# Optimization experiments

Hardware: AMD Instinct MI355X
Metric: run time of the kernel (lower is better)

The kernel has to match this reference:

```python
import jax, jax.numpy as jnp
import numpy as np

KH, KW, STRIDE = 5, 5, 1
OUT_CH = 64


def setup_inputs() -> dict:
    key = jax.random.key(0)
    k1, k2 = jax.random.split(key)
    x = jax.random.normal(k1, (16, 1, 256, 256), dtype=jnp.float32)
    # kaiming_uniform_(a=sqrt(5)) on fan_in=25 gives bound ~= sqrt(6/((1+5)*25)) ~= 0.2
    w = jax.random.uniform(k2, (OUT_CH, 1, KH, KW), dtype=jnp.float32, minval=-0.2, maxval=0.2)
    w = w.at[0].set(0.0)  # reset_parameters zeroes the first filter
    return {"x": x, "weight": w}


def reference(x, weight):
    """Faithful vectorized RBF_Conv2d forward.

    Original: for each output pixel (k,l), cdist between the flattened window
    (B, kh*kw) and flattened weights (O, kh*kw), std = sample std (ddof=1) of
    the (B,O) distance matrix, output = gauss(dist, std) = exp(-0.5*(d/std)^2).
    """
    B = x.shape[0]
    O = weight.shape[0]
    # im2col: (B, P=kh*kw, Ho, Wo), valid padding (in_channels == 1)
    patches = jax.lax.conv_general_dilated_patches(
        x, (KH, KW), (STRIDE, STRIDE), 'VALID')
    wf = weight.reshape(O, -1)                                  # (O, P)
    pn = jnp.sum(patches * patches, axis=1)                     # (B, Ho, Wo)
    wn = jnp.sum(wf * wf, axis=1)                               # (O,)
    cross = jnp.einsum('bphw,op->bohw', patches, wf)            # (B, O, Ho, Wo)
    d2 = pn[:, None] + wn[None, :, None, None] - 2.0 * cross
    dist = jnp.sqrt(jnp.maximum(d2, 1e-12))                     # euclidean cdist
    # per-output-pixel sample std (ddof=1) over the (B, O) distance matrix
    mean = jnp.mean(dist, axis=(0, 1), keepdims=True)           # (1,1,Ho,Wo)
    var = jnp.sum((dist - mean) ** 2, axis=(0, 1), keepdims=True) / (B * O - 1)
    std = jnp.sqrt(var)
    # gauss RBF
    return jnp.exp(-0.5 * (dist / std) ** 2)
```

## Files before the change

kernel.cpp:

```cpp
#include <hip/hip_runtime.h>

typedef float v2f __attribute__((ext_vector_type(2)));

#define KH 5
#define KW 5
#define HH 256
#define WW 256
#define HO 252
#define WO 252
#define NB 16
#define NO 64
#define PLANE (HO * WO)
#define NPASS 5
#define XC 85

__global__ __launch_bounds__(512, 4)
void rbf_conv2d_kernel(const float* __restrict__ x, const float* __restrict__ w,
                       float* __restrict__ out) {
    __shared__ float xs[NB][KH][XC];
    __shared__ float wn[NO];
    __shared__ float pS1[2][8][16];
    __shared__ float pS2[2][8][16];

    const int t  = threadIdx.x;
    const int k  = blockIdx.y;
    const int a0 = (4 * k) & 31;
    const int Le = a0 - 64 + 64 * (int)blockIdx.x;
    if (Le - 16 >= WO || Le + 64 <= 0) return;
    const int colbase = Le - 16;

    for (int idx = t; idx < NB * KH * XC; idx += 512) {
        int b   = idx / (KH * XC);
        int rem = idx - b * (KH * XC);
        int r   = rem / XC;
        int c   = rem - r * XC;
        int col = colbase + c;
        col = col < 0 ? 0 : (col > WW - 1 ? WW - 1 : col);
        xs[b][r][c] = x[(b * HH + k + r) * WW + col];
    }
    if (t < NO) {
        float s = 0.f;
        #pragma unroll
        for (int i = 0; i < 25; ++i) { float v = w[t * 25 + i]; s = fmaf(v, v, s); }
        wn[t] = s;
    }
    __syncthreads();

    const int p     = t & 15;
    const int b     = (t >> 4) & 15;
    const int obase = __builtin_amdgcn_readfirstlane((t >> 8) << 5);
    const int wv    = t >> 6;
    const int lane  = t & 63;
    const int bo_base = ((b * NO + obase) * HO + k) * WO;

    #pragma unroll 1
    for (int pi = 0; pi < NPASS; ++pi) {
        const int  Lp     = colbase + 16 * pi;
        const bool active = (Lp + 16 > 0) && (Lp < WO);
        const int  pb     = pi & 1;

        v2f   dv[16];
        float s1 = 0.f, s2 = 0.f;

        if (active) {
            float pr[25];
            float pn = 0.f;
            #pragma unroll
            for (int r = 0; r < KH; ++r)
                #pragma unroll
                for (int c = 0; c < KW; ++c) {
                    float v = xs[b][r][16 * pi + p + c];
                    pr[r * KW + c] = v;
                    pn = fmaf(v, v, pn);
                }
            v2f prv[12];
            #pragma unroll
            for (int i = 0; i < 12; ++i) { prv[i].x = pr[2 * i]; prv[i].y = pr[2 * i + 1]; }
            const float pr24 = pr[24];

            #pragma unroll
            for (int j = 0; j < 16; ++j) {
                float cr0, cr1;
                {
                    const float* __restrict__ wr = w + (obase + 2 * j) * 25;
                    v2f acc = {0.f, 0.f};
                    #pragma unroll
                    for (int i = 0; i < 12; ++i) {
                        v2f wv_; wv_.x = wr[2 * i]; wv_.y = wr[2 * i + 1];
                        acc = __builtin_elementwise_fma(prv[i], wv_, acc);
                    }
                    cr0 = acc.x + acc.y + pr24 * wr[24];
                }
                {
                    const float* __restrict__ wr = w + (obase + 2 * j + 1) * 25;
                    v2f acc = {0.f, 0.f};
                    #pragma unroll
                    for (int i = 0; i < 12; ++i) {
                        v2f wv_; wv_.x = wr[2 * i]; wv_.y = wr[2 * i + 1];
                        acc = __builtin_elementwise_fma(prv[i], wv_, acc);
                    }
                    cr1 = acc.x + acc.y + pr24 * wr[24];
                }
                float d20 = fmaxf(fmaf(-2.f, cr0, pn + wn[obase + 2 * j]),     1e-12f);
                float d21 = fmaxf(fmaf(-2.f, cr1, pn + wn[obase + 2 * j + 1]), 1e-12f);
                s2 += d20 + d21;
                dv[j].x = __builtin_amdgcn_sqrtf(d20);
                dv[j].y = __builtin_amdgcn_sqrtf(d21);
                s1 += dv[j].x + dv[j].y;
            }

            s1 += __shfl_xor(s1, 16); s2 += __shfl_xor(s2, 16);
            s1 += __shfl_xor(s1, 32); s2 += __shfl_xor(s2, 32);
            if (lane < 16) { pS1[pb][wv][lane] = s1; pS2[pb][wv][lane] = s2; }
        }
        __syncthreads();

        if (active) {
            float S1 = 0.f, S2 = 0.f;
            #pragma unroll
            for (int q = 0; q < 8; ++q) { S1 += pS1[pb][q][p]; S2 += pS2[pb][q][p]; }
            const float var  = (S2 - S1 * S1 * (1.0f / 1024.0f)) * (1.0f / 1023.0f);
            const float cinv = -0.72134752044448170368f / var;

            const int  l   = Lp + p;
            const bool ok  = (l >= 0) && (l < WO);
            const bool okE = ok && (pi >= 1);
            const bool okO = ok && (pi <= 3);
            v2f cv; cv.x = cinv; cv.y = cinv;
            const int base = bo_base + l;
            #pragma unroll
            for (int j = 0; j < 16; ++j) {
                v2f tt = dv[j] * dv[j];
                tt = tt * cv;
                float e0 = exp2f(tt.x);
                float e1 = exp2f(tt.y);
                if (okE) out[base + (2 * j) * PLANE]     = e0;
                if (okO) out[base + (2 * j + 1) * PLANE] = e1;
            }
        }
    }
}

extern "C" void kernel_launch(void* const* d_in, const int* in_sizes, int n_in,
                              void* d_out, int out_size, void* d_ws, size_t ws_size,
                              hipStream_t stream) {
    const float* x = (const float*)d_in[0];
    const float* w = (const float*)d_in[1];
    float* out = (float*)d_out;
    dim3 grid(6, HO);
    rbf_conv2d_kernel<<<grid, 512, 0, stream>>>(x, w, out);
}
```

Measured before the change: 349.5 us.

## Recompute distances in a second pass instead of holding them in registers

Restructures the kernel so each thread owns one output column across all 64 output channels and two batch elements, in place of the old 16-column passes. It makes two passes: the first computes the distance sums for the per-pixel std, and the second recomputes the 25-tap dot products and writes exp2 results directly. This removes the 16-entry distance register array and the overlapping passes with their partial writes, lowering register pressure and producing 64-lane contiguous stores. The cost is roughly double the FMA work for the cross terms and a different tile mapping with a smaller grid.

After: 340.2 us. -2.7%, faster.

```diff
diff --git a/kernel.cpp b/kernel.cpp
--- a/kernel.cpp
+++ b/kernel.cpp
@@ -11,30 +11,30 @@
 #define NB 16
 #define NO 64
 #define PLANE (HO * WO)
-#define NPASS 5
-#define XC 85
+#define TLW 64
+#define XCOLS (TLW + KW - 1)
 
 __global__ __launch_bounds__(512, 4)
 void rbf_conv2d_kernel(const float* __restrict__ x, const float* __restrict__ w,
                        float* __restrict__ out) {
-    __shared__ float xs[NB][KH][XC];
+    __shared__ float xs[NB][KH][XCOLS];
     __shared__ float wn[NO];
-    __shared__ float pS1[2][8][16];
-    __shared__ float pS2[2][8][16];
+    __shared__ float pS1[8][TLW];
+    __shared__ float pS2[8][TLW];
+    __shared__ float cinv_s[TLW];
 
-    const int t  = threadIdx.x;
-    const int k  = blockIdx.y;
-    const int a0 = (4 * k) & 31;
-    const int Le = a0 - 64 + 64 * (int)blockIdx.x;
-    if (Le - 16 >= WO || Le + 64 <= 0) return;
-    const int colbase = Le - 16;
+    const int t = threadIdx.x;
+    const int k = blockIdx.y;
+    const int a = (4 * k) & 15;
+    const int l0 = a - TLW + TLW * (int)blockIdx.x;
+    if (l0 >= WO || l0 + TLW <= 0) return;
 
-    for (int idx = t; idx < NB * KH * XC; idx += 512) {
-        int b   = idx / (KH * XC);
-        int rem = idx - b * (KH * XC);
-        int r   = rem / XC;
-        int c   = rem - r * XC;
-        int col = colbase + c;
+    for (int idx = t; idx < NB * KH * XCOLS; idx += 512) {
+        int b   = idx / (KH * XCOLS);
+        int rem = idx - b * (KH * XCOLS);
+        int r   = rem / XCOLS;
+        int c   = rem - r * XCOLS;
+        int col = l0 + c;
         col = col < 0 ? 0 : (col > WW - 1 ? WW - 1 : col);
         xs[b][r][c] = x[(b * HH + k + r) * WW + col];
     }
@@ -46,96 +46,124 @@
     }
     __syncthreads();
 
-    const int p     = t & 15;
-    const int b     = (t >> 4) & 15;
-    const int obase = __builtin_amdgcn_readfirstlane((t >> 8) << 5);
-    const int wv    = t >> 6;
-    const int lane  = t & 63;
-    const int bo_base = ((b * NO + obase) * HO + k) * WO;
+    const int lane = t & 63;
+    const int bg   = __builtin_amdgcn_readfirstlane(t >> 6);
+    const int l    = l0 + lane;
 
+    float s1 = 0.f, s2 = 0.f;
     #pragma unroll 1
-    for (int pi = 0; pi < NPASS; ++pi) {
-        const int  Lp     = colbase + 16 * pi;
-        const bool active = (Lp + 16 > 0) && (Lp < WO);
-        const int  pb     = pi & 1;
+    for (int bi = 0; bi < 2; ++bi) {
+        const int b = bg + 8 * bi;
+        float pr[25];
+        float pn = 0.f;
+        #pragma unroll
+        for (int r = 0; r < KH; ++r)
+            #pragma unroll
+            for (int c = 0; c < KW; ++c) {
+                float v = xs[b][r][lane + c];
+                pr[r * KW + c] = v;
+                pn = fmaf(v, v, pn);
+            }
+        v2f prv[12];
+        #pragma unroll
+        for (int i = 0; i < 12; ++i) { prv[i].x = pr[2 * i]; prv[i].y = pr[2 * i + 1]; }
+        const float pr24 = pr[24];
 
-        v2f   dv[16];
-        float s1 = 0.f, s2 = 0.f;
+        #pragma unroll 8
+        for (int j = 0; j < 32; ++j) {
+            float cr0, cr1;
+            {
+                const float* __restrict__ wr = w + (2 * j) * 25;
+                v2f acc = {0.f, 0.f};
+                #pragma unroll
+                for (int i = 0; i < 12; ++i) {
+                    v2f wv_; wv_.x = wr[2 * i]; wv_.y = wr[2 * i + 1];
+                    acc = __builtin_elementwise_fma(prv[i], wv_, acc);
+                }
+                cr0 = acc.x + acc.y + pr24 * wr[24];
+            }
+            {
+                const float* __restrict__ wr = w + (2 * j + 1) * 25;
+                v2f acc = {0.f, 0.f};
+                #pragma unroll
+                for (int i = 0; i < 12; ++i) {
+                    v2f wv_; wv_.x = wr[2 * i]; wv_.y = wr[2 * i + 1];
+                    acc = __builtin_elementwise_fma(prv[i], wv_, acc);
+                }
+                cr1 = acc.x + acc.y + pr24 * wr[24];
+            }
+            v2f wn2 = *(const v2f*)&wn[2 * j];
+            float d20 = fmaxf(fmaf(-2.f, cr0, pn + wn2.x), 1e-12f);
+            float d21 = fmaxf(fmaf(-2.f, cr1, pn + wn2.y), 1e-12f);
+            s2 += d20 + d21;
+            s1 += __builtin_amdgcn_sqrtf(d20) + __builtin_amdgcn_sqrtf(d21);
+        }
+    }
+    pS1[bg][lane] = s1;
+    pS2[bg][lane] = s2;
+    __syncthreads();
 
-        if (active) {
-            float pr[25];
-            float pn = 0.f;
+    if (t < TLW) {
+        float S1 = 0.f, S2 = 0.f;
+        #pragma unroll
+        for (int q = 0; q < 8; ++q) { S1 += pS1[q][t]; S2 += pS2[q][t]; }
+        const float var = (S2 - S1 * S1 * (1.0f / 1024.0f)) * (1.0f / 1023.0f);
+        cinv_s[t] = -0.72134752044448170368f / var;
+    }
+    __syncthreads();
+
+    const float ci  = cinv_s[lane];
+    const bool  ok  = ((unsigned)l < (unsigned)WO);
+    #pragma unroll 1
+    for (int bi = 0; bi < 2; ++bi) {
+        const int b = bg + 8 * bi;
+        float pr[25];
+        float pn = 0.f;
+        #pragma unroll
+        for (int r = 0; r < KH; ++r)
             #pragma unroll
-            for (int r = 0; r < KH; ++r)
+            for (int c = 0; c < KW; ++c) {
+                float v = xs[b][r][lane + c];
+                pr[r * KW + c] = v;
+                pn = fmaf(v, v, pn);
+            }
+        v2f prv[12];
+        #pragma unroll
+        for (int i = 0; i < 12; ++i) { prv[i].x = pr[2 * i]; prv[i].y = pr[2 * i + 1]; }
+        const float pr24 = pr[24];
+
+        const int base_b = (b * NO) * PLANE + k * WO + l;
+        #pragma unroll 8
+        for (int j = 0; j < 32; ++j) {
+            float cr0, cr1;
+            {
+                const float* __restrict__ wr = w + (2 * j) * 25;
+                v2f acc = {0.f, 0.f};
                 #pragma unroll
-                for (int c = 0; c < KW; ++c) {
-                    float v = xs[b][r][16 * pi + p + c];
-                    pr[r * KW + c] = v;
-                    pn = fmaf(v, v, pn);
+                for (int i = 0; i < 12; ++i) {
+                    v2f wv_; wv_.x = wr[2 * i]; wv_.y = wr[2 * i + 1];
+                    acc = __builtin_elementwise_fma(prv[i], wv_, acc);
                 }
-            v2f prv[12];
-            #pragma unroll
-            for (int i = 0; i < 12; ++i) { prv[i].x = pr[2 * i]; prv[i].y = pr[2 * i + 1]; }
-            const float pr24 = pr[24];
-
-            #pragma unroll
-            for (int j = 0; j < 16; ++j) {
-                float cr0, cr1;
-                {
-                    const float* __restrict__ wr = w + (obase + 2 * j) * 25;
-                    v2f acc = {0.f, 0.f};
-                    #pragma unroll
-                    for (int i = 0; i < 12; ++i) {
-                        v2f wv_; wv_.x = wr[2 * i]; wv_.y = wr[2 * i + 1];
-                        acc = __builtin_elementwise_fma(prv[i], wv_, acc);
-                    }
-                    cr0 = acc.x + acc.y + pr24 * wr[24];
+                cr0 = acc.x + acc.y + pr24 * wr[24];
+            }
+            {
+                const float* __restrict__ wr = w + (2 * j + 1) * 25;
+                v2f acc = {0.f, 0.f};
+                #pragma unroll
+                for (int i = 0; i < 12; ++i) {
+                    v2f wv_; wv_.x = wr[2 * i]; wv_.y = wr[2 * i + 1];
+                    acc = __builtin_elementwise_fma(prv[i], wv_, acc);
                 }
-                {
-                    const float* __restrict__ wr = w + (obase + 2 * j + 1) * 25;
-                    v2f acc = {0.f, 0.f};
-                    #pragma unroll
-                    for (int i = 0; i < 12; ++i) {
-                        v2f wv_; wv_.x = wr[2 * i]; wv_.y = wr[2 * i + 1];
-                        acc = __builtin_elementwise_fma(prv[i], wv_, acc);
-                    }
-                    cr1 = acc.x + acc.y + pr24 * wr[24];
-                }
-                float d20 = fmaxf(fmaf(-2.f, cr0, pn + wn[obase + 2 * j]),     1e-12f);
-                float d21 = fmaxf(fmaf(-2.f, cr1, pn + wn[obase + 2 * j + 1]), 1e-12f);
-                s2 += d20 + d21;
-                dv[j].x = __builtin_amdgcn_sqrtf(d20);
-                dv[j].y = __builtin_amdgcn_sqrtf(d21);
-                s1 += dv[j].x + dv[j].y;
+                cr1 = acc.x + acc.y + pr24 * wr[24];
             }
-
-            s1 += __shfl_xor(s1, 16); s2 += __shfl_xor(s2, 16);
-            s1 += __shfl_xor(s1, 32); s2 += __shfl_xor(s2, 32);
-            if (lane < 16) { pS1[pb][wv][lane] = s1; pS2[pb][wv][lane] = s2; }
-        }
-        __syncthreads();
-
-        if (active) {
-            float S1 = 0.f, S2 = 0.f;
-            #pragma unroll
-            for (int q = 0; q < 8; ++q) { S1 += pS1[pb][q][p]; S2 += pS2[pb][q][p]; }
-            const float var  = (S2 - S1 * S1 * (1.0f / 1024.0f)) * (1.0f / 1023.0f);
-            const float cinv = -0.72134752044448170368f / var;
-
-            const int  l   = Lp + p;
-            const bool ok  = (l >= 0) && (l < WO);
-            const bool okE = ok && (pi >= 1);
-            const bool okO = ok && (pi <= 3);
-            v2f cv; cv.x = cinv; cv.y = cinv;
-            const int base = bo_base + l;
-            #pragma unroll
-            for (int j = 0; j < 16; ++j) {
-                v2f tt = dv[j] * dv[j];
-                tt = tt * cv;
-                float e0 = exp2f(tt.x);
-                float e1 = exp2f(tt.y);
-                if (okE) out[base + (2 * j) * PLANE]     = e0;
-                if (okO) out[base + (2 * j + 1) * PLANE] = e1;
+            v2f wn2 = *(const v2f*)&wn[2 * j];
+            float d20 = fmaxf(fmaf(-2.f, cr0, pn + wn2.x), 1e-12f);
+            float d21 = fmaxf(fmaf(-2.f, cr1, pn + wn2.y), 1e-12f);
+            float e0 = exp2f(d20 * ci);
+            float e1 = exp2f(d21 * ci);
+            if (ok) {
+                out[base_b + (2 * j) * PLANE]     = e0;
+                out[base_b + (2 * j + 1) * PLANE] = e1;
             }
         }
     }
@@ -147,6 +175,6 @@
     const float* x = (const float*)d_in[0];
     const float* w = (const float*)d_in[1];
     float* out = (float*)d_out;
-    dim3 grid(6, HO);
+    dim3 grid(5, HO);
     rbf_conv2d_kernel<<<grid, 512, 0, stream>>>(x, w, out);
 }
```
